# Kernel optimization log

Measured on AMD Instinct MI355X. Metric: run time of the kernel, lower is better.

Reference implementation:

```python
import jax, jax.numpy as jnp
import numpy as np

B, S, D, H = 2, 2048, 1024, 16
HD = D // H  # head dim = 64


def setup_inputs() -> dict:
    key = jax.random.key(0)
    ks = jax.random.split(key, 9)
    sc = 1.0 / np.sqrt(D)
    x = jax.random.normal(ks[0], (B, S, D), dtype=jnp.float32)
    # weights stored as (in, out); y = x @ W + b (same math as torch Linear with W.T)
    Wq = jax.random.normal(ks[1], (D, D), dtype=jnp.float32) * sc
    Wk = jax.random.normal(ks[2], (D, D), dtype=jnp.float32) * sc
    Wv = jax.random.normal(ks[3], (D, D), dtype=jnp.float32) * sc
    Wo = jax.random.normal(ks[4], (D, D), dtype=jnp.float32) * sc
    bq = jax.random.normal(ks[5], (D,), dtype=jnp.float32) * 0.01
    bk = jax.random.normal(ks[6], (D,), dtype=jnp.float32) * 0.01
    bv = jax.random.normal(ks[7], (D,), dtype=jnp.float32) * 0.01
    bo = jax.random.normal(ks[8], (D,), dtype=jnp.float32) * 0.01
    return {"x": x, "Wq": Wq, "bq": bq, "Wk": Wk, "bk": bk,
            "Wv": Wv, "bv": bv, "Wo": Wo, "bo": bo}


def reference(x, Wq, bq, Wk, bk, Wv, bv, Wo, bo):
    b, s, d = x.shape
    q = (x @ Wq + bq).reshape(b, s, H, HD)
    k = (x @ Wk + bk).reshape(b, s, H, HD)
    v = (x @ Wv + bv).reshape(b, s, H, HD)
    # [b, h, s, s] scores, scaled by sqrt(head_dim)
    scores = jnp.einsum('bqhd,bkhd->bhqk', q, k) / np.sqrt(HD)
    causal = jnp.triu(jnp.ones((s, s), dtype=bool), k=1)  # True above diagonal
    scores = jnp.where(causal, -jnp.inf, scores)
    w = jax.nn.softmax(scores, axis=-1)  # dropout rate 0 -> identity
    ctx = jnp.einsum('bhqk,bkhd->bqhd', w, v).reshape(b, s, d)
    return ctx @ Wo + bo
```

## Files before the change

kernel.cpp:

```cpp
#include <hip/hip_runtime.h>
#include <math.h>

#define BB 2
#define SS 2048
#define DD 1024
#define HH 16
#define HDIM 64

typedef __bf16 bf16_t;
typedef __attribute__((ext_vector_type(8))) __bf16 bf16x8;
typedef __attribute__((ext_vector_type(4))) __bf16 bf16x4;
typedef __attribute__((ext_vector_type(4))) float f32x4;

__device__ inline bf16_t f2bf(float f) {
    unsigned int x; __builtin_memcpy(&x, &f, 4);
    unsigned int r = (x + 0x7FFFu + ((x >> 16) & 1u)) >> 16;
    unsigned short us = (unsigned short)r;
    bf16_t b; __builtin_memcpy(&b, &us, 2); return b;
}
__device__ inline unsigned int fbits(float f) {
    unsigned int x; __builtin_memcpy(&x, &f, 4); return x;
}
__device__ inline unsigned int pack_bf2(float a, float b) {
    return ((fbits(a) + 0x8000u) >> 16) | ((fbits(b) + 0x8000u) & 0xFFFF0000u);
}
__device__ inline void gload16(const void* g, void* lds_base) {
    __builtin_amdgcn_global_load_lds(
        (const __attribute__((address_space(1))) void*)g,
        (__attribute__((address_space(3))) void*)lds_base, 16, 0, 0);
}

__global__ __launch_bounds__(256)
void prep_kernel(const float* __restrict__ x, bf16_t* __restrict__ xb,
                 const float* __restrict__ W0, const float* __restrict__ W1,
                 const float* __restrict__ W2, const float* __restrict__ W3,
                 bf16x8* __restrict__ P0, bf16x8* __restrict__ P1,
                 bf16x8* __restrict__ P2, bf16x8* __restrict__ P3) {
    const int bid = blockIdx.x, tid = threadIdx.x;
    if (bid < 2048) {
        const int i = bid * 512 + tid;
        #pragma unroll
        for (int u = 0; u < 2; ++u) {
            const int j = i + u * 256;
            const float4 v = reinterpret_cast<const float4*>(x)[j];
            bf16x4 o;
            o.x = f2bf(v.x); o.y = f2bf(v.y); o.z = f2bf(v.z); o.w = f2bf(v.w);
            reinterpret_cast<bf16x4*>(xb)[j] = o;
        }
    } else {
        const int t = (bid - 2048) * 256 + tid;
        const int g = t >> 10, n = t & 1023;
        const float* Ws[4] = {W0, W1, W2, W3};
        bf16x8* Pp[4] = {P0, P1, P2, P3};
        #pragma unroll
        for (int m = 0; m < 4; ++m) {
            bf16x8 v;
            #pragma unroll
            for (int j = 0; j < 8; ++j) v[j] = f2bf(Ws[m][(size_t)(g * 8 + j) * DD + n]);
            Pp[m][(size_t)g * DD + n] = v;
        }
    }
}

__global__ __launch_bounds__(256)
void gemm_qkv(const bf16_t* __restrict__ A,
              const bf16x8* __restrict__ Wp0, const bf16x8* __restrict__ Wp1,
              const bf16x8* __restrict__ Wp2,
              const float* __restrict__ b0, const float* __restrict__ b1,
              const float* __restrict__ b2,
              bf16_t* __restrict__ C0, bf16_t* __restrict__ C1,
              bf16_t* __restrict__ Vt) {
    __shared__ bf16x8 smem_v[4096];
    char* const smem = (char*)smem_v;

    const int f = blockIdx.x;
    const int xcd = f & 7, l = f >> 3;
    const int ytile = xcd * 4 + (l & 3);
    const int zx = l >> 2;
    const int z = zx >> 3;
    const int xtile = zx & 7;

    const bf16x8* Wp = (z == 0) ? Wp0 : (z == 1) ? Wp1 : Wp2;
    const float* bias = (z == 0) ? b0 : (z == 1) ? b1 : b2;

    const int tid = threadIdx.x;
    const int ln = tid & 63, wv = tid >> 6;
    const int quad = ln >> 4, l15 = ln & 15;
    const int wr = wv >> 1, wc = wv & 1;
    const int m0 = ytile * 128;
    const int n0 = xtile * 128;

    int arow[4], acl[4], bg[4], bn[4];
    #pragma unroll
    for (int u = 0; u < 4; ++u) {
        const int S = (wv * 4 + u) * 64 + ln;
        arow[u] = S >> 3; acl[u] = (S & 7) ^ (arow[u] & 7);
        bg[u] = S >> 7;   bn[u] = S & 127;
    }

    f32x4 acc[4][4];
    #pragma unroll
    for (int i = 0; i < 4; ++i)
        #pragma unroll
        for (int j = 0; j < 4; ++j) acc[i][j] = (f32x4){0.f, 0.f, 0.f, 0.f};

    auto stage = [&](int t, int buf) {
        char* const base = smem + buf * 32768;
        const int k0 = t * 64, kg0 = t * 8;
        #pragma unroll
        for (int u = 0; u < 4; ++u) {
            gload16(&A[(size_t)(m0 + arow[u]) * DD + k0 + acl[u] * 8],
                    base + (size_t)(wv * 4 + u) * 1024);
            gload16(&Wp[(size_t)(kg0 + bg[u]) * DD + n0 + bn[u]],
                    base + 16384 + (size_t)(wv * 4 + u) * 1024);
        }
    };

    auto body = [&](int buf, int tnext, int dostage) {
        const bf16x8 (*As)[8]   = reinterpret_cast<const bf16x8(*)[8]>(smem + buf * 32768);
        const bf16x8 (*Bs)[128] = reinterpret_cast<const bf16x8(*)[128]>(smem + buf * 32768 + 16384);
        bf16x8 fa[2][4], fb[2][4];
        #pragma unroll
        for (int kk = 0; kk < 2; ++kk) {
            #pragma unroll
            for (int mi = 0; mi < 4; ++mi) {
                const int row = wr * 64 + mi * 16 + l15;
                fa[kk][mi] = As[row][(kk * 4 + quad) ^ (row & 7)];
            }
            #pragma unroll
            for (int ni = 0; ni < 4; ++ni)
                fb[kk][ni] = Bs[kk * 4 + quad][wc * 64 + ni * 16 + l15];
        }
        if (dostage) stage(tnext, buf ^ 1);
        #pragma unroll
        for (int kk = 0; kk < 2; ++kk)
            #pragma unroll
            for (int mi = 0; mi < 4; ++mi)
                #pragma unroll
                for (int ni = 0; ni < 4; ++ni)
                    acc[mi][ni] = __builtin_amdgcn_mfma_f32_16x16x32_bf16(
                        fa[kk][mi], fb[kk][ni], acc[mi][ni], 0, 0, 0);
    };

    stage(0, 0);
    __syncthreads();
    #pragma unroll
    for (int th = 0; th < 8; ++th) {
        body(0, 2 * th + 1, 1);
        __syncthreads();
        body(1, 2 * th + 2, th < 7);
        if (th < 7) __syncthreads();
    }

    if (z < 2) {
        bf16_t* C = (z == 0) ? C0 : C1;
        #pragma unroll
        for (int ni = 0; ni < 4; ++ni) {
            const int col = n0 + wc * 64 + ni * 16 + l15;
            const float bv = bias[col];
            #pragma unroll
            for (int mi = 0; mi < 4; ++mi)
                #pragma unroll
                for (int r = 0; r < 4; ++r) {
                    const int row = m0 + wr * 64 + mi * 16 + quad * 4 + r;
                    C[(size_t)row * DD + col] = f2bf(acc[mi][ni][r] + bv);
                }
        }
    } else {
        unsigned short (*T)[136] = reinterpret_cast<unsigned short(*)[136]>(smem);
        __syncthreads();
        #pragma unroll
        for (int ni = 0; ni < 4; ++ni) {
            const int cl = wc * 64 + ni * 16 + l15;
            const float bv = bias[n0 + cl];
            #pragma unroll
            for (int mi = 0; mi < 4; ++mi) {
                const int rl = wr * 64 + mi * 16 + quad * 4;
                uint2 pk;
                pk.x = pack_bf2(acc[mi][ni][0] + bv, acc[mi][ni][1] + bv);
                pk.y = pack_bf2(acc[mi][ni][2] + bv, acc[mi][ni][3] + bv);
                *reinterpret_cast<uint2*>(&T[cl][rl]) = pk;
            }
        }
        __syncthreads();
        const int b = m0 >> 11, s0 = m0 & 2047, h0 = n0 >> 6;
        #pragma unroll
        for (int u = 0; u < 8; ++u) {
            const int c = u * 256 + tid;
            const int s8 = c & 15, nl = c >> 4;
            const bf16x8 v = *reinterpret_cast<const bf16x8*>(&T[nl][s8 * 8]);
            const int bh = b * 16 + h0 + (nl >> 6), d = nl & 63;
            *reinterpret_cast<bf16x8*>(
                &Vt[((size_t)bh * 64 + d) * SS + s0 + s8 * 8]) = v;
        }
    }
}

__global__ __launch_bounds__(256)
void gemm_out(const bf16_t* __restrict__ A, const bf16x8* __restrict__ Wp,
              const float* __restrict__ bias, float* __restrict__ C) {
    __shared__ bf16x8 As[2][128][8];
    __shared__ bf16x8 Bs[2][8][64];

    const int f = blockIdx.x;
    const int xcd = f & 7, l = f >> 3;
    const int ytile = xcd * 4 + (l & 3);
    const int xtile = l >> 2;

    const int tid = threadIdx.x;
    const int ln = tid & 63, wv = tid >> 6;
    const int quad = ln >> 4, l15 = ln & 15;
    const int wr = wv >> 1, wc = wv & 1;
    const int m0 = ytile * 128;
    const int n0 = xtile * 64;

    int arow[4], acl[4], bkg[2], bn[2];
    #pragma unroll
    for (int u = 0; u < 4; ++u) {
        const int S = (wv * 4 + u) * 64 + ln;
        arow[u] = S >> 3; acl[u] = (S & 7) ^ (arow[u] & 7);
    }
    #pragma unroll
    for (int u = 0; u < 2; ++u) {
        const int S = (wv * 2 + u) * 64 + ln;
        bkg[u] = S >> 6; bn[u] = S & 63;
    }

    f32x4 acc[4][2];
    #pragma unroll
    for (int i = 0; i < 4; ++i)
        #pragma unroll
        for (int j = 0; j < 2; ++j) acc[i][j] = (f32x4){0.f, 0.f, 0.f, 0.f};

    auto stage = [&](int t, int buf) {
        const int k0 = t * 64, kg0 = t * 8;
        #pragma unroll
        for (int u = 0; u < 4; ++u)
            gload16(&A[(size_t)(m0 + arow[u]) * DD + k0 + acl[u] * 8],
                    (char*)&As[buf][0][0] + (size_t)(wv * 4 + u) * 1024);
        #pragma unroll
        for (int u = 0; u < 2; ++u)
            gload16(&Wp[(size_t)(kg0 + bkg[u]) * DD + n0 + bn[u]],
                    (char*)&Bs[buf][0][0] + (size_t)(wv * 2 + u) * 1024);
    };

    auto body = [&](int buf, int tnext, int dostage) {
        bf16x8 fa[2][4], fb[2][2];
        #pragma unroll
        for (int kk = 0; kk < 2; ++kk) {
            #pragma unroll
            for (int mi = 0; mi < 4; ++mi) {
                const int row = wr * 64 + mi * 16 + l15;
                fa[kk][mi] = As[buf][row][(kk * 4 + quad) ^ (row & 7)];
            }
            #pragma unroll
            for (int ni = 0; ni < 2; ++ni)
                fb[kk][ni] = Bs[buf][kk * 4 + quad][wc * 32 + ni * 16 + l15];
        }
        if (dostage) stage(tnext, buf ^ 1);
        #pragma unroll
        for (int kk = 0; kk < 2; ++kk)
            #pragma unroll
            for (int mi = 0; mi < 4; ++mi)
                #pragma unroll
                for (int ni = 0; ni < 2; ++ni)
                    acc[mi][ni] = __builtin_amdgcn_mfma_f32_16x16x32_bf16(
                        fa[kk][mi], fb[kk][ni], acc[mi][ni], 0, 0, 0);
    };

    stage(0, 0);
    __syncthreads();
    #pragma unroll
    for (int th = 0; th < 8; ++th) {
        body(0, 2 * th + 1, 1);
        __syncthreads();
        body(1, 2 * th + 2, th < 7);
        if (th < 7) __syncthreads();
    }

    #pragma unroll
    for (int ni = 0; ni < 2; ++ni) {
        const int col = n0 + wc * 32 + ni * 16 + l15;
        const float bv = bias[col];
        #pragma unroll
        for (int mi = 0; mi < 4; ++mi)
            #pragma unroll
            for (int r = 0; r < 4; ++r) {
                const int row = m0 + wr * 64 + mi * 16 + quad * 4 + r;
                C[(size_t)row * DD + col] = acc[mi][ni][r] + bv;
            }
    }
}

#define SCL 0.18033688f
#define FM  12.0f

__global__ __launch_bounds__(256)
void attn_mfma(const bf16_t* __restrict__ Q, const bf16_t* __restrict__ Kg,
               const bf16_t* __restrict__ Vt, bf16_t* __restrict__ Ctx) {
    __shared__ bf16x8 Ks[2][64][8];
    __shared__ bf16x8 Vs[2][64][8];
    __shared__ unsigned short Ps[4][16][64];

    const int tid = threadIdx.x;
    const int ln = tid & 63, w = tid >> 6;
    const int quad = ln >> 4, l15 = ln & 15;

    const int f = blockIdx.x;
    const int xcd = f & 7, l = f >> 3;
    const int bh = xcd * 4 + (l & 3);
    const int ytile = l >> 2;
    const int tswz = (bh + ytile) & 15;
    const int qt = (ytile < 16) ? tswz : 31 - tswz;

    const int b = bh >> 4, h = bh & 15;
    const size_t rowbase = (size_t)b * SS;
    const int col0 = h * 64;

    const int krow0 = w * 16 + (ln >> 3);
    const int krow1 = krow0 + 8;
    const int kc0 = (ln & 7) ^ (krow0 & 7);
    const int kc1 = (ln & 7) ^ (krow1 & 7);

    bf16x8 fq[2];
    const int qrow = qt * 64 + w * 16 + l15;
    #pragma unroll
    for (int kk = 0; kk < 2; ++kk)
        fq[kk] = *reinterpret_cast<const bf16x8*>(
            &Q[(rowbase + qrow) * DD + col0 + kk * 32 + quad * 8]);

    f32x4 acc_o[4];
    #pragma unroll
    for (int i = 0; i < 4; ++i) acc_o[i] = (f32x4){0.f, 0.f, 0.f, 0.f};
    float lsum = 0.f;

    const bf16_t* kp0 = &Kg[(rowbase + krow0) * DD + col0 + kc0 * 8];
    const bf16_t* kp1 = &Kg[(rowbase + krow1) * DD + col0 + kc1 * 8];
    const bf16_t* vp0 = &Vt[((size_t)bh * 64 + krow0) * SS + kc0 * 8];
    const bf16_t* vp1 = &Vt[((size_t)bh * 64 + krow1) * SS + kc1 * 8];

    auto stageadv = [&](int buf) {
        char* kb = (char*)Ks + buf * 8192 + w * 2048;
        char* vb = (char*)Vs + buf * 8192 + w * 2048;
        gload16(kp0, kb);
        gload16(kp1, kb + 1024);
        gload16(vp0, vb);
        gload16(vp1, vb + 1024);
        kp0 += 64 * DD; kp1 += 64 * DD;
        vp0 += 64;      vp1 += 64;
    };

    const int swz = l15 & 7;

    auto compute_tile = [&](int buf, int dq) {
        unsigned short* const psw = &Ps[w][l15][0];
        #pragma unroll
        for (int ni = 0; ni < 4; ++ni) {
            const int slot = ni * 4 + quad;
            unsigned short* pdst = psw + (((slot >> 1) ^ swz) * 8 + (slot & 1) * 4);
            const int g = ni * 16;
            if (g > dq) {
                *reinterpret_cast<uint2*>(pdst) = (uint2){0u, 0u};
                continue;
            }
            f32x4 st = (f32x4){0.f, 0.f, 0.f, 0.f};
            const int krow = ni * 16 + l15;
            #pragma unroll
            for (int kk = 0; kk < 2; ++kk) {
                const bf16x8 fk = Ks[buf][krow][(kk * 4 + quad) ^ (krow & 7)];
                st = __builtin_amdgcn_mfma_f32_16x16x32_bf16(fk, fq[kk], st, 0, 0, 0);
            }
            float p[4];
            #pragma unroll
            for (int r = 0; r < 4; ++r) {
                p[r] = __builtin_amdgcn_exp2f(st[r] * SCL - FM);
                if (g == dq && (quad * 4 + r) > l15) p[r] = 0.f;
            }
            lsum += (p[0] + p[1]) + (p[2] + p[3]);
            uint2 pk;
            pk.x = pack_bf2(p[0], p[1]);
            pk.y = pack_bf2(p[2], p[3]);
            *reinterpret_cast<uint2*>(pdst) = pk;
        }
        __builtin_amdgcn_s_setprio(1);
        #pragma unroll
        for (int kk = 0; kk < 2; ++kk) {
            const bf16x8 fp = *reinterpret_cast<const bf16x8*>(
                &Ps[w][l15][(((kk * 4 + quad) ^ swz) * 8)]);
            #pragma unroll
            for (int nd = 0; nd < 4; ++nd) {
                const int vrow = nd * 16 + l15;
                const bf16x8 fv = Vs[buf][vrow][(kk * 4 + quad) ^ (vrow & 7)];
                acc_o[nd] = __builtin_amdgcn_mfma_f32_16x16x32_bf16(fv, fp, acc_o[nd], 0, 0, 0);
            }
        }
        __builtin_amdgcn_s_setprio(0);
    };

    stageadv(0);
    __syncthreads();
    int t = 0;
    while (t + 2 <= qt) {
        stageadv(1);
        compute_tile(0, 112);
        __syncthreads();
        stageadv(0);
        compute_tile(1, 112);
        __syncthreads();
        t += 2;
    }
    if (t < qt) {
        stageadv(1);
        compute_tile(0, 112);
        __syncthreads();
        compute_tile(1, w * 16);
    } else {
        compute_tile(0, w * 16);
    }

    {
        float s = lsum;
        s += __shfl_xor(s, 16);
        s += __shfl_xor(s, 32);
        const float inv = 1.f / s;
        const size_t orow = (rowbase + qrow) * DD + col0;
        #pragma unroll
        for (int nd = 0; nd < 4; ++nd) {
            uint2 ov;
            ov.x = pack_bf2(acc_o[nd][0] * inv, acc_o[nd][1] * inv);
            ov.y = pack_bf2(acc_o[nd][2] * inv, acc_o[nd][3] * inv);
            *reinterpret_cast<uint2*>(&Ctx[orow + nd * 16 + quad * 4]) = ov;
        }
    }
}

extern "C" void kernel_launch(void* const* d_in, const int* in_sizes, int n_in,
                              void* d_out, int out_size, void* d_ws, size_t ws_size,
                              hipStream_t stream) {
    const float* x  = (const float*)d_in[0];
    const float* Wq = (const float*)d_in[1];
    const float* bq = (const float*)d_in[2];
    const float* Wk = (const float*)d_in[3];
    const float* bk = (const float*)d_in[4];
    const float* Wv = (const float*)d_in[5];
    const float* bv = (const float*)d_in[6];
    const float* Wo = (const float*)d_in[7];
    const float* bo = (const float*)d_in[8];
    float* out = (float*)d_out;

    const size_t M = (size_t)BB * SS;
    const size_t mat = M * DD;
    const size_t wsz = (size_t)DD * DD;

    bf16_t* ws = (bf16_t*)d_ws;
    bf16_t* xb   = ws;
    bf16_t* Wqp  = ws + mat;
    bf16_t* Wkp  = Wqp + wsz;
    bf16_t* Wvp  = Wkp + wsz;
    bf16_t* Wop  = Wvp + wsz;
    bf16_t* Qb   = Wop + wsz;
    bf16_t* Kb   = Qb + mat;
    bf16_t* Vtb  = Kb + mat;
    bf16_t* Ctxb = Vtb + mat;

    dim3 blk(256);
    hipLaunchKernelGGL(prep_kernel, dim3(2560), blk, 0, stream,
                       x, xb, Wq, Wk, Wv, Wo,
                       (bf16x8*)Wqp, (bf16x8*)Wkp, (bf16x8*)Wvp, (bf16x8*)Wop);

    hipLaunchKernelGGL(gemm_qkv, dim3(768), blk, 0, stream,
                       xb, (const bf16x8*)Wqp, (const bf16x8*)Wkp, (const bf16x8*)Wvp,
                       bq, bk, bv, Qb, Kb, Vtb);

    hipLaunchKernelGGL(attn_mfma, dim3(1024), blk, 0, stream,
                       Qb, Kb, Vtb, Ctxb);

    hipLaunchKernelGGL(gemm_out, dim3(512), blk, 0, stream,
                       Ctxb, (const bf16x8*)Wop, bo, out);
}
```

Before: 179.5 us.

## Triple-buffer GEMM K-loop, fold softmax scale into Q, use hardware bf16 pack

Both projection GEMMs move from a double-buffered loop over 64-wide K-steps to a triple-buffered loop over 32-wide K-steps. Each iteration prefetches two steps ahead and uses explicit vmcnt waits plus raw barriers instead of __syncthreads. The softmax scale is folded into the Q projection epilogue, and the max offset now seeds the MFMA accumulator, which removes a multiply-subtract per score. The software bf16 pack is replaced with the v_cvt_pk_bf16_f32 instruction, which adds rounding differences and relies on hand-tuned wait counts being correct.

```diff
diff --git a/kernel.cpp b/kernel.cpp
--- a/kernel.cpp
+++ b/kernel.cpp
@@ -18,17 +18,19 @@
     unsigned short us = (unsigned short)r;
     bf16_t b; __builtin_memcpy(&b, &us, 2); return b;
 }
-__device__ inline unsigned int fbits(float f) {
-    unsigned int x; __builtin_memcpy(&x, &f, 4); return x;
-}
-__device__ inline unsigned int pack_bf2(float a, float b) {
-    return ((fbits(a) + 0x8000u) >> 16) | ((fbits(b) + 0x8000u) & 0xFFFF0000u);
+__device__ inline unsigned int cvtpk(float a, float b) {
+    unsigned int r;
+    asm("v_cvt_pk_bf16_f32 %0, %1, %2" : "=v"(r) : "v"(a), "v"(b));
+    return r;
 }
 __device__ inline void gload16(const void* g, void* lds_base) {
     __builtin_amdgcn_global_load_lds(
         (const __attribute__((address_space(1))) void*)g,
         (__attribute__((address_space(3))) void*)lds_base, 16, 0, 0);
 }
+
+#define SCL 0.18033688f
+#define FM  12.0f
 
 __global__ __launch_bounds__(256)
 void prep_kernel(const float* __restrict__ x, bf16_t* __restrict__ xb,
@@ -70,7 +72,7 @@
               const float* __restrict__ b2,
               bf16_t* __restrict__ C0, bf16_t* __restrict__ C1,
               bf16_t* __restrict__ Vt) {
-    __shared__ bf16x8 smem_v[4096];
+    __shared__ bf16x8 smem_v[3072];
     char* const smem = (char*)smem_v;
 
     const int f = blockIdx.x;
@@ -90,11 +92,11 @@
     const int m0 = ytile * 128;
     const int n0 = xtile * 128;
 
-    int arow[4], acl[4], bg[4], bn[4];
-    #pragma unroll
-    for (int u = 0; u < 4; ++u) {
-        const int S = (wv * 4 + u) * 64 + ln;
-        arow[u] = S >> 3; acl[u] = (S & 7) ^ (arow[u] & 7);
+    int arow[2], acl[2], bg[2], bn[2];
+    #pragma unroll
+    for (int u = 0; u < 2; ++u) {
+        const int S = (wv * 2 + u) * 64 + ln;
+        arow[u] = S >> 2; acl[u] = (S & 3) ^ (arow[u] & 3);
         bg[u] = S >> 7;   bn[u] = S & 127;
     }
 
@@ -105,55 +107,51 @@
         for (int j = 0; j < 4; ++j) acc[i][j] = (f32x4){0.f, 0.f, 0.f, 0.f};
 
     auto stage = [&](int t, int buf) {
-        char* const base = smem + buf * 32768;
-        const int k0 = t * 64, kg0 = t * 8;
-        #pragma unroll
-        for (int u = 0; u < 4; ++u) {
+        char* const base = smem + buf * 16384;
+        const int k0 = t * 32, kg0 = t * 4;
+        #pragma unroll
+        for (int u = 0; u < 2; ++u) {
             gload16(&A[(size_t)(m0 + arow[u]) * DD + k0 + acl[u] * 8],
-                    base + (size_t)(wv * 4 + u) * 1024);
+                    base + (wv * 2 + u) * 1024);
             gload16(&Wp[(size_t)(kg0 + bg[u]) * DD + n0 + bn[u]],
-                    base + 16384 + (size_t)(wv * 4 + u) * 1024);
+                    base + 8192 + (wv * 2 + u) * 1024);
         }
     };
 
-    auto body = [&](int buf, int tnext, int dostage) {
-        const bf16x8 (*As)[8]   = reinterpret_cast<const bf16x8(*)[8]>(smem + buf * 32768);
-        const bf16x8 (*Bs)[128] = reinterpret_cast<const bf16x8(*)[128]>(smem + buf * 32768 + 16384);
-        bf16x8 fa[2][4], fb[2][4];
-        #pragma unroll
-        for (int kk = 0; kk < 2; ++kk) {
-            #pragma unroll
-            for (int mi = 0; mi < 4; ++mi) {
-                const int row = wr * 64 + mi * 16 + l15;
-                fa[kk][mi] = As[row][(kk * 4 + quad) ^ (row & 7)];
-            }
+    stage(0, 0);
+    stage(1, 1);
+    asm volatile("s_waitcnt vmcnt(4)" ::: "memory");
+    __builtin_amdgcn_s_barrier();
+
+    #pragma unroll
+    for (int t = 0; t < 32; ++t) {
+        const int bsel = t % 3;
+        const bf16x8 (*As)[4]   = reinterpret_cast<const bf16x8(*)[4]>(smem + bsel * 16384);
+        const bf16x8 (*Bs)[128] = reinterpret_cast<const bf16x8(*)[128]>(smem + bsel * 16384 + 8192);
+        bf16x8 fa[4], fb[4];
+        #pragma unroll
+        for (int mi = 0; mi < 4; ++mi) {
+            const int row = wr * 64 + mi * 16 + l15;
+            fa[mi] = As[row][quad ^ (row & 3)];
+        }
+        #pragma unroll
+        for (int ni = 0; ni < 4; ++ni)
+            fb[ni] = Bs[quad][wc * 64 + ni * 16 + l15];
+        if (t + 2 < 32) stage(t + 2, (t + 2) % 3);
+        #pragma unroll
+        for (int mi = 0; mi < 4; ++mi)
             #pragma unroll
             for (int ni = 0; ni < 4; ++ni)
-                fb[kk][ni] = Bs[kk * 4 + quad][wc * 64 + ni * 16 + l15];
-        }
-        if (dostage) stage(tnext, buf ^ 1);
-        #pragma unroll
-        for (int kk = 0; kk < 2; ++kk)
-            #pragma unroll
-            for (int mi = 0; mi < 4; ++mi)
-                #pragma unroll
-                for (int ni = 0; ni < 4; ++ni)
-                    acc[mi][ni] = __builtin_amdgcn_mfma_f32_16x16x32_bf16(
-                        fa[kk][mi], fb[kk][ni], acc[mi][ni], 0, 0, 0);
-    };
-
-    stage(0, 0);
-    __syncthreads();
-    #pragma unroll
-    for (int th = 0; th < 8; ++th) {
-        body(0, 2 * th + 1, 1);
-        __syncthreads();
-        body(1, 2 * th + 2, th < 7);
-        if (th < 7) __syncthreads();
+                acc[mi][ni] = __builtin_amdgcn_mfma_f32_16x16x32_bf16(
+                    fa[mi], fb[ni], acc[mi][ni], 0, 0, 0);
+        if (t < 30)       asm volatile("s_waitcnt vmcnt(4)" ::: "memory");
+        else if (t == 30) asm volatile("s_waitcnt vmcnt(0)" ::: "memory");
+        if (t < 31) __builtin_amdgcn_s_barrier();
     }
 
     if (z < 2) {
         bf16_t* C = (z == 0) ? C0 : C1;
+        const float sc = (z == 0) ? SCL : 1.0f;
         #pragma unroll
         for (int ni = 0; ni < 4; ++ni) {
             const int col = n0 + wc * 64 + ni * 16 + l15;
@@ -163,7 +161,7 @@
                 #pragma unroll
                 for (int r = 0; r < 4; ++r) {
                     const int row = m0 + wr * 64 + mi * 16 + quad * 4 + r;
-                    C[(size_t)row * DD + col] = f2bf(acc[mi][ni][r] + bv);
+                    C[(size_t)row * DD + col] = f2bf((acc[mi][ni][r] + bv) * sc);
                 }
         }
     } else {
@@ -177,8 +175,8 @@
             for (int mi = 0; mi < 4; ++mi) {
                 const int rl = wr * 64 + mi * 16 + quad * 4;
                 uint2 pk;
-                pk.x = pack_bf2(acc[mi][ni][0] + bv, acc[mi][ni][1] + bv);
-                pk.y = pack_bf2(acc[mi][ni][2] + bv, acc[mi][ni][3] + bv);
+                pk.x = cvtpk(acc[mi][ni][0] + bv, acc[mi][ni][1] + bv);
+                pk.y = cvtpk(acc[mi][ni][2] + bv, acc[mi][ni][3] + bv);
                 *reinterpret_cast<uint2*>(&T[cl][rl]) = pk;
             }
         }
@@ -199,8 +197,8 @@
 __global__ __launch_bounds__(256)
 void gemm_out(const bf16_t* __restrict__ A, const bf16x8* __restrict__ Wp,
               const float* __restrict__ bias, float* __restrict__ C) {
-    __shared__ bf16x8 As[2][128][8];
-    __shared__ bf16x8 Bs[2][8][64];
+    __shared__ bf16x8 smem_v[2304];
+    char* const smem = (char*)smem_v;
 
     const int f = blockIdx.x;
     const int xcd = f & 7, l = f >> 3;
@@ -214,17 +212,14 @@
     const int m0 = ytile * 128;
     const int n0 = xtile * 64;
 
-    int arow[4], acl[4], bkg[2], bn[2];
-    #pragma unroll
-    for (int u = 0; u < 4; ++u) {
-        const int S = (wv * 4 + u) * 64 + ln;
-        arow[u] = S >> 3; acl[u] = (S & 7) ^ (arow[u] & 7);
-    }
+    int arow[2], acl[2];
     #pragma unroll
     for (int u = 0; u < 2; ++u) {
         const int S = (wv * 2 + u) * 64 + ln;
-        bkg[u] = S >> 6; bn[u] = S & 63;
-    }
+        arow[u] = S >> 2; acl[u] = (S & 3) ^ (arow[u] & 3);
+    }
+    const int Sb = wv * 64 + ln;
+    const int bkg = Sb >> 6, bnn = Sb & 63;
 
     f32x4 acc[4][2];
     #pragma unroll
@@ -233,49 +228,45 @@
         for (int j = 0; j < 2; ++j) acc[i][j] = (f32x4){0.f, 0.f, 0.f, 0.f};
 
     auto stage = [&](int t, int buf) {
-        const int k0 = t * 64, kg0 = t * 8;
-        #pragma unroll
-        for (int u = 0; u < 4; ++u)
+        char* const base = smem + buf * 12288;
+        const int k0 = t * 32, kg0 = t * 4;
+        #pragma unroll
+        for (int u = 0; u < 2; ++u)
             gload16(&A[(size_t)(m0 + arow[u]) * DD + k0 + acl[u] * 8],
-                    (char*)&As[buf][0][0] + (size_t)(wv * 4 + u) * 1024);
-        #pragma unroll
-        for (int u = 0; u < 2; ++u)
-            gload16(&Wp[(size_t)(kg0 + bkg[u]) * DD + n0 + bn[u]],
-                    (char*)&Bs[buf][0][0] + (size_t)(wv * 2 + u) * 1024);
+                    base + (wv * 2 + u) * 1024);
+        gload16(&Wp[(size_t)(kg0 + bkg) * DD + n0 + bnn],
+                base + 8192 + wv * 1024);
     };
 
-    auto body = [&](int buf, int tnext, int dostage) {
-        bf16x8 fa[2][4], fb[2][2];
-        #pragma unroll
-        for (int kk = 0; kk < 2; ++kk) {
-            #pragma unroll
-            for (int mi = 0; mi < 4; ++mi) {
-                const int row = wr * 64 + mi * 16 + l15;
-                fa[kk][mi] = As[buf][row][(kk * 4 + quad) ^ (row & 7)];
-            }
+    stage(0, 0);
+    stage(1, 1);
+    asm volatile("s_waitcnt vmcnt(3)" ::: "memory");
+    __builtin_amdgcn_s_barrier();
+
+    #pragma unroll
+    for (int t = 0; t < 32; ++t) {
+        const int bsel = t % 3;
+        const bf16x8 (*As)[4]  = reinterpret_cast<const bf16x8(*)[4]>(smem + bsel * 12288);
+        const bf16x8 (*Bs)[64] = reinterpret_cast<const bf16x8(*)[64]>(smem + bsel * 12288 + 8192);
+        bf16x8 fa[4], fb[2];
+        #pragma unroll
+        for (int mi = 0; mi < 4; ++mi) {
+            const int row = wr * 64 + mi * 16 + l15;
+            fa[mi] = As[row][quad ^ (row & 3)];
+        }
+        #pragma unroll
+        for (int ni = 0; ni < 2; ++ni)
+            fb[ni] = Bs[quad][wc * 32 + ni * 16 + l15];
+        if (t + 2 < 32) stage(t + 2, (t + 2) % 3);
+        #pragma unroll
+        for (int mi = 0; mi < 4; ++mi)
             #pragma unroll
             for (int ni = 0; ni < 2; ++ni)
-                fb[kk][ni] = Bs[buf][kk * 4 + quad][wc * 32 + ni * 16 + l15];
-        }
-        if (dostage) stage(tnext, buf ^ 1);
-        #pragma unroll
-        for (int kk = 0; kk < 2; ++kk)
-            #pragma unroll
-            for (int mi = 0; mi < 4; ++mi)
-                #pragma unroll
-                for (int ni = 0; ni < 2; ++ni)
-                    acc[mi][ni] = __builtin_amdgcn_mfma_f32_16x16x32_bf16(
-                        fa[kk][mi], fb[kk][ni], acc[mi][ni], 0, 0, 0);
-    };
-
-    stage(0, 0);
-    __syncthreads();
-    #pragma unroll
-    for (int th = 0; th < 8; ++th) {
-        body(0, 2 * th + 1, 1);
-        __syncthreads();
-        body(1, 2 * th + 2, th < 7);
-        if (th < 7) __syncthreads();
+                acc[mi][ni] = __builtin_amdgcn_mfma_f32_16x16x32_bf16(
+                    fa[mi], fb[ni], acc[mi][ni], 0, 0, 0);
+        if (t < 30)       asm volatile("s_waitcnt vmcnt(3)" ::: "memory");
+        else if (t == 30) asm volatile("s_waitcnt vmcnt(0)" ::: "memory");
+        if (t < 31) __builtin_amdgcn_s_barrier();
     }
 
     #pragma unroll
@@ -291,9 +282,6 @@
             }
     }
 }
-
-#define SCL 0.18033688f
-#define FM  12.0f
 
 __global__ __launch_bounds__(256)
 void attn_mfma(const bf16_t* __restrict__ Q, const bf16_t* __restrict__ Kg,
@@ -363,7 +351,7 @@
                 *reinterpret_cast<uint2*>(pdst) = (uint2){0u, 0u};
                 continue;
             }
-            f32x4 st = (f32x4){0.f, 0.f, 0.f, 0.f};
+            f32x4 st = (f32x4){-FM, -FM, -FM, -FM};
             const int krow = ni * 16 + l15;
             #pragma unroll
             for (int kk = 0; kk < 2; ++kk) {
@@ -373,13 +361,13 @@
             float p[4];
             #pragma unroll
             for (int r = 0; r < 4; ++r) {
-                p[r] = __builtin_amdgcn_exp2f(st[r] * SCL - FM);
+                p[r] = __builtin_amdgcn_exp2f(st[r]);
                 if (g == dq && (quad * 4 + r) > l15) p[r] = 0.f;
             }
             lsum += (p[0] + p[1]) + (p[2] + p[3]);
             uint2 pk;
-            pk.x = pack_bf2(p[0], p[1]);
-            pk.y = pack_bf2(p[2], p[3]);
+            pk.x = cvtpk(p[0], p[1]);
+            pk.y = cvtpk(p[2], p[3]);
             *reinterpret_cast<uint2*>(pdst) = pk;
         }
         __builtin_amdgcn_s_setprio(1);
@@ -427,8 +415,8 @@
         #pragma unroll
         for (int nd = 0; nd < 4; ++nd) {
             uint2 ov;
-            ov.x = pack_bf2(acc_o[nd][0] * inv, acc_o[nd][1] * inv);
-            ov.y = pack_bf2(acc_o[nd][2] * inv, acc_o[nd][3] * inv);
+            ov.x = cvtpk(acc_o[nd][0] * inv, acc_o[nd][1] * inv);
+            ov.y = cvtpk(acc_o[nd][2] * inv, acc_o[nd][3] * inv);
             *reinterpret_cast<uint2*>(&Ctx[orow + nd * 16 + quad * 4]) = ov;
         }
     }
```

Measured after the change: 169.6 us. 1.06x faster.
